# Performance work log

Measured on AMD Instinct MI355X. Metric: run time of the kernel, lower is better.

Reference implementation:

```python
import math
import jax, jax.numpy as jnp
import numpy as np

N_EMBD = 1024
N_HEAD = 16
N_QUERY_SETS = 4
B, T = 8, 1024


def setup_inputs() -> dict:
    key = jax.random.key(0)
    kx, kw1, kw2 = jax.random.split(key, 3)
    C = N_EMBD
    x = jax.random.normal(kx, (B, T, C), dtype=jnp.float32)
    # torch Linear weights are [out_features, in_features]
    W_attn = jax.random.normal(kw1, ((N_QUERY_SETS + 2) * C, C), dtype=jnp.float32) * (1.0 / math.sqrt(C))
    W_proj = jax.random.normal(kw2, (C, N_QUERY_SETS * C), dtype=jnp.float32) * (1.0 / math.sqrt(N_QUERY_SETS * C))
    return {"x": x, "W_attn": W_attn, "W_proj": W_proj}


def reference(x, W_attn, W_proj):
    Bz, Tz, C = x.shape
    hd = C // N_HEAD
    scale = 1.0 / math.sqrt(hd)
    qkv = x @ W_attn.T                       # [B,T,(nqs+2)*C]
    parts = jnp.split(qkv, N_QUERY_SETS + 2, axis=-1)
    k = parts[-2].reshape(Bz, Tz, N_HEAD, hd).transpose(0, 2, 1, 3)  # [B,H,T,hd]
    v = parts[-1].reshape(Bz, Tz, N_HEAD, hd).transpose(0, 2, 1, 3)
    causal = jnp.tril(jnp.ones((Tz, Tz), dtype=bool))
    outs = []
    for g in range(N_QUERY_SETS):  # fixed small structural loop, reuses K/V
        q = parts[g].reshape(Bz, Tz, N_HEAD, hd).transpose(0, 2, 1, 3)
        att = jnp.einsum('bhqd,bhkd->bhqk', q, k) * scale
        att = jnp.where(causal, att, -jnp.inf)
        att = jax.nn.softmax(att, axis=-1)
        y = jnp.einsum('bhqk,bhkd->bhqd', att, v)
        outs.append(y.transpose(0, 2, 1, 3).reshape(Bz, Tz, C))
    combined = jnp.concatenate(outs, axis=-1)  # [B,T,nqs*C]
    return combined @ W_proj.T                 # [B,T,C]
```

## Files before the change

kernel.cpp:

```cpp
#include <hip/hip_runtime.h>


#define DEVI __device__ __forceinline__

typedef __attribute__((ext_vector_type(4)))  float f32x4;
typedef __attribute__((ext_vector_type(16))) float f32x16;
typedef __attribute__((ext_vector_type(8)))  short bf16x8;

static DEVI short f2bf(float f) {
    union { float f; unsigned int i; } c; c.f = f;
    unsigned int i = c.i;
    unsigned int r = i + 0x7FFFu + ((i >> 16) & 1u);
    return (short)(r >> 16);
}

static DEVI unsigned pk2bf(float a, float b) {
    return __builtin_amdgcn_perm(__float_as_uint(b), __float_as_uint(a), 0x07060302u);
}

static DEVI void gload16(const void* g, void* l) {
    __builtin_amdgcn_global_load_lds(
        (const __attribute__((address_space(1))) unsigned int*)g,
        (__attribute__((address_space(3))) unsigned int*)l,
        16, 0, 0);
}

#define BARRIER() do { __builtin_amdgcn_s_barrier(); \
                       __builtin_amdgcn_sched_barrier(0); } while (0)
#define WAITVM(n) do { asm volatile("s_waitcnt vmcnt(%0)" :: "i"(n) : "memory"); \
                       __builtin_amdgcn_sched_barrier(0); } while (0)

__global__ __launch_bounds__(256)
void cvt_all(const float* __restrict__ x, const float* __restrict__ Wa,
             short* __restrict__ dst, float qs) {
    const int i = blockIdx.x * 256 + threadIdx.x;
    const int X8 = 1048576, WQ8 = 524288;
    const float* src;
    float scale = 1.0f;
    if (i < X8) {
        src = x + (size_t)i * 8;
    } else {
        int j = i - X8;
        src = Wa + (size_t)j * 8;
        if (j < WQ8) scale = qs;
    }
    const float4* p = (const float4*)src;
    float4 v0 = p[0], v1 = p[1];
    short r[8] = { f2bf(v0.x * scale), f2bf(v0.y * scale),
                   f2bf(v0.z * scale), f2bf(v0.w * scale),
                   f2bf(v1.x * scale), f2bf(v1.y * scale),
                   f2bf(v1.z * scale), f2bf(v1.w * scale) };
    *(uint4*)(dst + (size_t)i * 8) = *(uint4*)r;
}

__global__ __launch_bounds__(256)
void cvt_bf16(const float* __restrict__ in, short* __restrict__ out, int n8,
              float scale) {
    int i = blockIdx.x * 256 + threadIdx.x;
    if (i >= n8) return;
    const float4* p = (const float4*)in + (size_t)i * 2;
    float4 v0 = p[0], v1 = p[1];
    short r[8] = { f2bf(v0.x * scale), f2bf(v0.y * scale),
                   f2bf(v0.z * scale), f2bf(v0.w * scale),
                   f2bf(v1.x * scale), f2bf(v1.y * scale),
                   f2bf(v1.z * scale), f2bf(v1.w * scale) };
    *(uint4*)(out + (size_t)i * 8) = *(uint4*)r;
}

static DEVI void stage_half(const short* __restrict__ G, int ldg,
                            short* ldsHalf, int tid) {
    #pragma unroll
    for (int i = 0; i < 2; ++i) {
        int c = tid + (i << 9);
        int row = c >> 3;
        int k8 = (c & 7) ^ (row & 7);
        gload16(G + (size_t)row * ldg + k8 * 8, ldsHalf + ((c >> 6) << 9));
    }
}

static DEVI bf16x8 ldsfrag(const short* half, int lr, int k8r) {
    int off = lr * 64 + ((k8r ^ (lr & 7)) << 3);
    return *(const bf16x8*)(half + off);
}

__global__ __launch_bounds__(512)
void gemm8_bt(const short* __restrict__ A, const short* __restrict__ B,
              short* __restrict__ C, int M, int N, int K, int nwgN) {
    __shared__ short lds[65536];
    short* const ldsA = lds;
    short* const ldsB = lds + 32768;

    const int tid  = threadIdx.x;
    const int lane = tid & 63;
    const int w    = tid >> 6;
    const int wr   = w >> 2;
    const int wc   = w & 3;
    const int l15  = lane & 15;
    const int g4   = lane >> 4;

    const int nwg = gridDim.x;
    const int wg  = blockIdx.x;
    const int swz = (wg & 7) * (nwg >> 3) + (wg >> 3);
    const int tm  = swz / nwgN, tn = swz % nwgN;

    const short* Ag = A + (size_t)tm * 256 * K;
    const short* Bg = B + (size_t)tn * 256 * K;
    const int NT = K >> 6;

    f32x4 acc[8][4] = {};

    stage_half(Ag,                      K, ldsA,               tid);
    stage_half(Ag + (size_t)128 * K,    K, ldsA + 8192,        tid);
    stage_half(Bg,                      K, ldsB,               tid);
    stage_half(Bg + (size_t)128 * K,    K, ldsB + 8192,        tid);
    stage_half(Bg + 64,                 K, ldsB + 16384,       tid);
    stage_half(Bg + (size_t)128 * K + 64, K, ldsB + 16384 + 8192, tid);
    WAITVM(4);
    BARRIER();

    for (int u = 0; u < NT; ++u) {
        const int buf = u & 1;
        const short* Ah = ldsA + buf * 16384 + wr * 8192;
        const short* Bh = ldsB + buf * 16384 + (wc >> 1) * 8192;
        const int lrB = (wc & 1) * 64;
        short* stA = ldsA + (buf ^ 1) * 16384;
        short* stB = ldsB + buf * 16384;
        const short* AgN  = Ag + (size_t)(u + 1) * 64;
        const short* BgN2 = Bg + (size_t)(u + 2) * 64;
        const bool doA = (u + 1 < NT), doB = (u + 2 < NT);

        bf16x8 af[4][2], b0[2][2], b1[2][2];

        #pragma unroll
        for (int f = 0; f < 4; ++f)
            #pragma unroll
            for (int ks = 0; ks < 2; ++ks)
                af[f][ks] = ldsfrag(Ah, f * 16 + l15, ks * 4 + g4);
        #pragma unroll
        for (int fn = 0; fn < 2; ++fn)
            #pragma unroll
            for (int ks = 0; ks < 2; ++ks)
                b0[fn][ks] = ldsfrag(Bh, lrB + fn * 16 + l15, ks * 4 + g4);
        if (doA) stage_half(AgN, K, stA, tid);
        BARRIER();
        __builtin_amdgcn_s_setprio(1);
        #pragma unroll
        for (int f = 0; f < 4; ++f)
            #pragma unroll
            for (int fn = 0; fn < 2; ++fn)
                #pragma unroll
                for (int ks = 0; ks < 2; ++ks)
                    acc[f][fn] = __builtin_amdgcn_mfma_f32_16x16x32_bf16(
                        af[f][ks], b0[fn][ks], acc[f][fn], 0, 0, 0);
        __builtin_amdgcn_s_setprio(0);
        BARRIER();

        #pragma unroll
        for (int fn = 0; fn < 2; ++fn)
            #pragma unroll
            for (int ks = 0; ks < 2; ++ks)
                b1[fn][ks] = ldsfrag(Bh, lrB + 32 + fn * 16 + l15, ks * 4 + g4);
        if (doA) stage_half(AgN + (size_t)128 * K, K, stA + 8192, tid);
        BARRIER();
        __builtin_amdgcn_s_setprio(1);
        #pragma unroll
        for (int f = 0; f < 4; ++f)
            #pragma unroll
            for (int fn = 0; fn < 2; ++fn)
                #pragma unroll
                for (int ks = 0; ks < 2; ++ks)
                    acc[f][2 + fn] = __builtin_amdgcn_mfma_f32_16x16x32_bf16(
                        af[f][ks], b1[fn][ks], acc[f][2 + fn], 0, 0, 0);
        __builtin_amdgcn_s_setprio(0);
        BARRIER();

        #pragma unroll
        for (int f = 0; f < 4; ++f)
            #pragma unroll
            for (int ks = 0; ks < 2; ++ks)
                af[f][ks] = ldsfrag(Ah, 64 + f * 16 + l15, ks * 4 + g4);
        if (doB) stage_half(BgN2, K, stB, tid);
        BARRIER();
        __builtin_amdgcn_s_setprio(1);
        #pragma unroll
        for (int f = 0; f < 4; ++f)
            #pragma unroll
            for (int fn = 0; fn < 2; ++fn)
                #pragma unroll
                for (int ks = 0; ks < 2; ++ks)
                    acc[4 + f][fn] = __builtin_amdgcn_mfma_f32_16x16x32_bf16(
                        af[f][ks], b0[fn][ks], acc[4 + f][fn], 0, 0, 0);
        __builtin_amdgcn_s_setprio(0);
        BARRIER();

        if (doB) stage_half(BgN2 + (size_t)128 * K, K, stB + 8192, tid);
        BARRIER();
        __builtin_amdgcn_s_setprio(1);
        #pragma unroll
        for (int f = 0; f < 4; ++f)
            #pragma unroll
            for (int fn = 0; fn < 2; ++fn)
                #pragma unroll
                for (int ks = 0; ks < 2; ++ks)
                    acc[4 + f][2 + fn] = __builtin_amdgcn_mfma_f32_16x16x32_bf16(
                        af[f][ks], b1[fn][ks], acc[4 + f][2 + fn], 0, 0, 0);
        __builtin_amdgcn_s_setprio(0);
        if (doB) { WAITVM(4); } else { WAITVM(0); }
        BARRIER();
    }

    const size_t r0 = (size_t)tm * 256 + wr * 128 + g4 * 4;
    const int    c0 = tn * 256 + wc * 64 + l15;
    #pragma unroll
    for (int mf = 0; mf < 8; ++mf)
        #pragma unroll
        for (int nf = 0; nf < 4; ++nf)
            #pragma unroll
            for (int j = 0; j < 4; ++j)
                C[(r0 + mf * 16 + j) * N + c0 + nf * 16] = f2bf(acc[mf][nf][j]);
}

__global__ __launch_bounds__(512)
void gemm8_bt2(const short* __restrict__ A, const short* __restrict__ B,
               float* __restrict__ C, int M, int N, int K) {
    __shared__ short lds[49152];
    short* const ldsA = lds;
    short* const ldsB = lds + 32768;

    const int tid  = threadIdx.x;
    const int lane = tid & 63;
    const int w    = tid >> 6;
    const int wr   = w >> 2;
    const int wc   = w & 3;
    const int l15  = lane & 15;
    const int g4   = lane >> 4;

    const int nwg = gridDim.x;
    const int wg  = blockIdx.x;
    const int swz = (wg & 7) * (nwg >> 3) + (wg >> 3);
    const int tm  = swz >> 3, tn = swz & 7;

    const short* Ag = A + (size_t)tm * 256 * K;
    const short* Bg = B + (size_t)tn * 128 * K;
    const int NT = K >> 6;

    f32x4 acc[8][2] = {};

    stage_half(Ag,                   K, ldsA,        tid);
    stage_half(Ag + (size_t)128 * K, K, ldsA + 8192, tid);
    stage_half(Bg,                   K, ldsB,        tid);
    stage_half(Bg + 64,              K, ldsB + 8192, tid);
    WAITVM(2);
    BARRIER();

    for (int u = 0; u < NT; ++u) {
        const int buf = u & 1;
        const short* Ah = ldsA + buf * 16384 + wr * 8192;
        const short* Bb = ldsB + buf * 8192;
        short* stA = ldsA + (buf ^ 1) * 16384;
        short* stB = ldsB + buf * 8192;
        const short* AgN  = Ag + (size_t)(u + 1) * 64;
        const short* BgN2 = Bg + (size_t)(u + 2) * 64;
        const bool doA = (u + 1 < NT), doB = (u + 2 < NT);

        bf16x8 af[4][2], b[2][2];

        #pragma unroll
        for (int f = 0; f < 4; ++f)
            #pragma unroll
            for (int ks = 0; ks < 2; ++ks)
                af[f][ks] = ldsfrag(Ah, f * 16 + l15, ks * 4 + g4);
        #pragma unroll
        for (int fn = 0; fn < 2; ++fn)
            #pragma unroll
            for (int ks = 0; ks < 2; ++ks)
                b[fn][ks] = ldsfrag(Bb, wc * 32 + fn * 16 + l15, ks * 4 + g4);
        if (doA) stage_half(AgN, K, stA, tid);
        BARRIER();
        __builtin_amdgcn_s_setprio(1);
        #pragma unroll
        for (int f = 0; f < 4; ++f)
            #pragma unroll
            for (int fn = 0; fn < 2; ++fn)
                #pragma unroll
                for (int ks = 0; ks < 2; ++ks)
                    acc[f][fn] = __builtin_amdgcn_mfma_f32_16x16x32_bf16(
                        af[f][ks], b[fn][ks], acc[f][fn], 0, 0, 0);
        __builtin_amdgcn_s_setprio(0);
        BARRIER();

        #pragma unroll
        for (int f = 0; f < 4; ++f)
            #pragma unroll
            for (int ks = 0; ks < 2; ++ks)
                af[f][ks] = ldsfrag(Ah, 64 + f * 16 + l15, ks * 4 + g4);
        if (doA) stage_half(AgN + (size_t)128 * K, K, stA + 8192, tid);
        if (doB) stage_half(BgN2, K, stB, tid);
        BARRIER();
        __builtin_amdgcn_s_setprio(1);
        #pragma unroll
        for (int f = 0; f < 4; ++f)
            #pragma unroll
            for (int fn = 0; fn < 2; ++fn)
                #pragma unroll
                for (int ks = 0; ks < 2; ++ks)
                    acc[4 + f][fn] = __builtin_amdgcn_mfma_f32_16x16x32_bf16(
                        af[f][ks], b[fn][ks], acc[4 + f][fn], 0, 0, 0);
        __builtin_amdgcn_s_setprio(0);
        if (doB) { WAITVM(2); } else { WAITVM(0); }
        BARRIER();
    }

    const size_t r0 = (size_t)tm * 256 + wr * 128 + g4 * 4;
    const int    c0 = tn * 128 + wc * 32 + l15;
    #pragma unroll
    for (int mf = 0; mf < 8; ++mf)
        #pragma unroll
        for (int nf = 0; nf < 2; ++nf)
            #pragma unroll
            for (int j = 0; j < 4; ++j)
                C[(r0 + mf * 16 + j) * N + c0 + nf * 16] = acc[mf][nf][j];
}

__global__ __launch_bounds__(512, 4)
void attn_fwd(const short* __restrict__ qkv, short* __restrict__ Y) {
    __shared__ __align__(16) char smem[34816];
    short* const KsB0 = (short*)smem;
    short* const VtB0 = (short*)smem + 4096;
    short* const KsB1 = (short*)smem + 8192;
    short* const VtB1 = (short*)smem + 12288;

    const int tid  = threadIdx.x;
    const int lane = tid & 63;
    const int w    = tid >> 6;
    const int q    = lane & 31;
    const int hf   = lane >> 5;

    const int b  = blockIdx.x >> 4;
    const int h  = blockIdx.x & 15;
    const int qt = (gridDim.y - 1) - blockIdx.y;
    const int g  = w >> 1;
    const int lq = (w & 1) * 32 + q;
    const size_t RS = 6144;
    const int bT = b * 1024;

    bf16x8 qf[4];
    {
        const short* qp = qkv + (size_t)(bT + qt * 64 + lq) * RS + g * 1024 + h * 64 + 8 * hf;
        #pragma unroll
        for (int ks2 = 0; ks2 < 4; ks2++)
            qf[ks2] = *(const bf16x8*)(qp + 16 * ks2);
    }

    f32x16 ot[2] = {};
    float lsum = 0.f;

    const int kvS   = tid >> 3;
    const int klog  = (tid & 7) ^ (kvS & 7);
    const int d2    = tid >> 4;
    const int ch4   = tid & 15;
    const int vd0   = d2 * 2;
    const int vp0   = (ch4 >> 1) ^ (vd0 & 7);
    const int vp1   = (ch4 >> 1) ^ ((vd0 + 1) & 7);

    const short* const kvtile = qkv + (size_t)bT * RS + h * 64;

    {
        const short* vp = kvtile + (size_t)(ch4 * 4) * RS + 5120 + vd0;
        unsigned v0 = *(const unsigned*)(vp);
        unsigned v1 = *(const unsigned*)(vp + RS);
        unsigned v2 = *(const unsigned*)(vp + 2 * RS);
        unsigned v3 = *(const unsigned*)(vp + 3 * RS);
        gload16(kvtile + (size_t)kvS * RS + 4096 + klog * 8, KsB0 + w * 512);
        uint2 lo, hi2;
        lo.x  = __builtin_amdgcn_perm(v1, v0, 0x05040100u);
        lo.y  = __builtin_amdgcn_perm(v3, v2, 0x05040100u);
        hi2.x = __builtin_amdgcn_perm(v1, v0, 0x07060302u);
        hi2.y = __builtin_amdgcn_perm(v3, v2, 0x07060302u);
        char* vb = (char*)VtB0;
        *(uint2*)(vb + vd0 * 128 + vp0 * 16 + (ch4 & 1) * 8)       = lo;
        *(uint2*)(vb + (vd0 + 1) * 128 + vp1 * 16 + (ch4 & 1) * 8) = hi2;
    }
    __syncthreads();

    for (int kvt = 0; kvt <= qt; kvt++) {
        short* const Ksc = (kvt & 1) ? KsB1 : KsB0;
        short* const Vtc = (kvt & 1) ? VtB1 : VtB0;
        short* const Ksn = (kvt & 1) ? KsB0 : KsB1;
        short* const Vtn = (kvt & 1) ? VtB0 : VtB1;
        const bool pf = (kvt < qt);

        unsigned v0, v1, v2, v3;
        if (pf) {
            const short* vp = kvtile + (size_t)((kvt + 1) * 64 + ch4 * 4) * RS + 5120 + vd0;
            v0 = *(const unsigned*)(vp);
            v1 = *(const unsigned*)(vp + RS);
            v2 = *(const unsigned*)(vp + 2 * RS);
            v3 = *(const unsigned*)(vp + 3 * RS);
            gload16(kvtile + (size_t)((kvt + 1) * 64 + kvS) * RS + 4096 + klog * 8,
                    Ksn + w * 512);
        }

        f32x16 stt[2] = {};
        __builtin_amdgcn_s_setprio(1);
        #pragma unroll
        for (int sti = 0; sti < 2; sti++) {
            const int kvr = sti * 32 + q;
            #pragma unroll
            for (int ks2 = 0; ks2 < 4; ks2++) {
                const int phys = (2 * ks2 + hf) ^ (kvr & 7);
                bf16x8 kf = *(const bf16x8*)(Ksc + kvr * 64 + phys * 8);
                stt[sti] = __builtin_amdgcn_mfma_f32_32x32x16_bf16(kf, qf[ks2], stt[sti], 0, 0, 0);
            }
        }
        __builtin_amdgcn_s_setprio(0);

        if (kvt == qt) {
            #pragma unroll
            for (int sti = 0; sti < 2; sti++)
                #pragma unroll
                for (int r = 0; r < 16; r++) {
                    int kvl = sti * 32 + (r & 3) + 8 * (r >> 2) + 4 * hf;
                    if (kvl > lq) stt[sti][r] = -3e38f;
                }
        }

        float sp[4] = { 0.f, 0.f, 0.f, 0.f };
        #pragma unroll
        for (int sti = 0; sti < 2; sti++)
            #pragma unroll
            for (int r = 0; r < 16; r++) {
                float e = __builtin_amdgcn_exp2f(stt[sti][r]);
                stt[sti][r] = e;
                sp[r & 3] += e;
            }
        float sum = (sp[0] + sp[1]) + (sp[2] + sp[3]);
        sum += __shfl_xor(sum, 32);
        lsum += sum;

        if (pf) {
            uint2 lo, hi2;
            lo.x  = __builtin_amdgcn_perm(v1, v0, 0x05040100u);
            lo.y  = __builtin_amdgcn_perm(v3, v2, 0x05040100u);
            hi2.x = __builtin_amdgcn_perm(v1, v0, 0x07060302u);
            hi2.y = __builtin_amdgcn_perm(v3, v2, 0x07060302u);
            char* vb = (char*)Vtn;
            *(uint2*)(vb + vd0 * 128 + vp0 * 16 + (ch4 & 1) * 8)       = lo;
            *(uint2*)(vb + (vd0 + 1) * 128 + vp1 * 16 + (ch4 & 1) * 8) = hi2;
        }

        bf16x8 pf4[4];
        #pragma unroll
        for (int ks = 0; ks < 4; ks++) {
            const int sti = ks >> 1, base = 8 * (ks & 1);
            unsigned X0 = pk2bf(stt[sti][base + 0], stt[sti][base + 1]);
            unsigned X1 = pk2bf(stt[sti][base + 2], stt[sti][base + 3]);
            unsigned Y0 = pk2bf(stt[sti][base + 4], stt[sti][base + 5]);
            unsigned Y1 = pk2bf(stt[sti][base + 6], stt[sti][base + 7]);
            asm("v_permlane32_swap_b32 %0, %1" : "+v"(X0), "+v"(Y0));
            asm("v_permlane32_swap_b32 %0, %1" : "+v"(X1), "+v"(Y1));
            unsigned t[4] = { X0, X1, Y0, Y1 };
            pf4[ks] = *(bf16x8*)t;
        }

        __builtin_amdgcn_s_setprio(1);
        #pragma unroll
        for (int dsub = 0; dsub < 2; dsub++) {
            const int dr = dsub * 32 + q;
            #pragma unroll
            for (int ks = 0; ks < 4; ks++) {
                const int phys = (2 * ks + hf) ^ (dr & 7);
                bf16x8 vf = *(const bf16x8*)(Vtc + dr * 64 + phys * 8);
                ot[dsub] = __builtin_amdgcn_mfma_f32_32x32x16_bf16(vf, pf4[ks], ot[dsub], 0, 0, 0);
            }
        }
        __builtin_amdgcn_s_setprio(0);

        __syncthreads();
    }

    unsigned* obuf = (unsigned*)smem;
    const float inv = 1.0f / lsum;
    const int SQ = g * 64 + lq;
    #pragma unroll
    for (int dsub = 0; dsub < 2; dsub++)
        #pragma unroll
        for (int r = 0; r < 16; r += 2) {
            int d = dsub * 32 + (r & 3) + 8 * (r >> 2) + 4 * hf;
            unsigned pk = ((unsigned)(unsigned short)f2bf(ot[dsub][r] * inv)) |
                          (((unsigned)(unsigned short)f2bf(ot[dsub][r + 1] * inv)) << 16);
            obuf[SQ * 34 + (d >> 1)] = pk;
        }
    __syncthreads();
    {
        const int SQ2 = tid >> 1, seg = tid & 1;
        const int g2 = SQ2 >> 6, lq2 = SQ2 & 63;
        const size_t row = (size_t)(bT + qt * 64 + lq2);
        const unsigned* src = obuf + SQ2 * 34 + seg * 16;
        unsigned* dst = (unsigned*)(Y + row * 4096 + g2 * 1024 + h * 64 + seg * 32);
        #pragma unroll
        for (int k = 0; k < 4; k++) {
            uint2 u0 = *(const uint2*)(src + 4 * k);
            uint2 u1 = *(const uint2*)(src + 4 * k + 2);
            uint4 t; t.x = u0.x; t.y = u0.y; t.z = u1.x; t.w = u1.y;
            *(uint4*)(dst + 4 * k) = t;
        }
    }
}

extern "C" void kernel_launch(void* const* d_in, const int* in_sizes, int n_in,
                              void* d_out, int out_size, void* d_ws, size_t ws_size,
                              hipStream_t stream) {
    const float* x  = (const float*)d_in[0];
    const float* Wa = (const float*)d_in[1];
    const float* Wp = (const float*)d_in[2];
    float* out = (float*)d_out;

    short* qkv = (short*)d_ws;
    short* Yb  = qkv + (size_t)8192 * 6144;
    short* xb  = Yb;
    short* Wab = Yb + (size_t)8192 * 1024;
    short* Wpb = qkv;

    const float QS = 0.18033688011112042f;
    dim3 blk(256);
    cvt_all<<<dim3((8192 + 6144) * 1024 / 8 / 256), blk, 0, stream>>>(x, Wa, xb, QS);
    gemm8_bt<<<dim3(768), dim3(512), 0, stream>>>(xb, Wab, qkv, 8192, 6144, 1024, 24);
    attn_fwd<<<dim3(128, 16), dim3(512), 0, stream>>>(qkv, Yb);
    cvt_bf16<<<dim3(1024 * 4096 / 8 / 256), blk, 0, stream>>>(Wp, Wpb, 1024 * 4096 / 8, 1.0f);
    gemm8_bt2<<<dim3(256), dim3(512), 0, stream>>>(Yb, Wpb, out, 8192, 1024, 4096);
}
```

Baseline: 313.8 us.

## Process two KV tiles per barrier with four-stage LDS ring buffer

Reworks the attention KV loop from double buffering with one barrier per 64-key tile to a 4-slot LDS ring. Two tiles are computed per iteration and the next two are prefetched, which halves the number of __syncthreads calls and gives loads more time to land. The cost is LDS use rising from about 34 KB to 64 KB, which may limit the 4-blocks-per-CU occupancy, and more registers held live for the staged V values.

```diff
diff --git a/kernel.cpp b/kernel.cpp
--- a/kernel.cpp
+++ b/kernel.cpp
@@ -324,11 +324,7 @@
 
 __global__ __launch_bounds__(512, 4)
 void attn_fwd(const short* __restrict__ qkv, short* __restrict__ Y) {
-    __shared__ __align__(16) char smem[34816];
-    short* const KsB0 = (short*)smem;
-    short* const VtB0 = (short*)smem + 4096;
-    short* const KsB1 = (short*)smem + 8192;
-    short* const VtB1 = (short*)smem + 12288;
+    __shared__ __align__(16) char smem[65536];
 
     const int tid  = threadIdx.x;
     const int lane = tid & 63;
@@ -343,6 +339,7 @@
     const int lq = (w & 1) * 32 + q;
     const size_t RS = 6144;
     const int bT = b * 1024;
+    const int NT = qt + 1;
 
     bf16x8 qf[4];
     {
@@ -365,42 +362,33 @@
 
     const short* const kvtile = qkv + (size_t)bT * RS + h * 64;
 
-    {
-        const short* vp = kvtile + (size_t)(ch4 * 4) * RS + 5120 + vd0;
-        unsigned v0 = *(const unsigned*)(vp);
-        unsigned v1 = *(const unsigned*)(vp + RS);
-        unsigned v2 = *(const unsigned*)(vp + 2 * RS);
-        unsigned v3 = *(const unsigned*)(vp + 3 * RS);
-        gload16(kvtile + (size_t)kvS * RS + 4096 + klog * 8, KsB0 + w * 512);
+    auto Ks = [&](int t) { return (short*)smem + (t & 3) * 8192; };
+    auto Vt = [&](int t) { return (short*)smem + (t & 3) * 8192 + 4096; };
+
+    auto kstage = [&](int t) {
+        gload16(kvtile + (size_t)(t * 64 + kvS) * RS + 4096 + klog * 8,
+                Ks(t) + w * 512);
+    };
+    auto vload = [&](int t, unsigned* gg) {
+        const short* vp = kvtile + (size_t)(t * 64 + ch4 * 4) * RS + 5120 + vd0;
+        gg[0] = *(const unsigned*)(vp);
+        gg[1] = *(const unsigned*)(vp + RS);
+        gg[2] = *(const unsigned*)(vp + 2 * RS);
+        gg[3] = *(const unsigned*)(vp + 3 * RS);
+    };
+    auto vwrite = [&](int t, const unsigned* gg) {
         uint2 lo, hi2;
-        lo.x  = __builtin_amdgcn_perm(v1, v0, 0x05040100u);
-        lo.y  = __builtin_amdgcn_perm(v3, v2, 0x05040100u);
-        hi2.x = __builtin_amdgcn_perm(v1, v0, 0x07060302u);
-        hi2.y = __builtin_amdgcn_perm(v3, v2, 0x07060302u);
-        char* vb = (char*)VtB0;
+        lo.x  = __builtin_amdgcn_perm(gg[1], gg[0], 0x05040100u);
+        lo.y  = __builtin_amdgcn_perm(gg[3], gg[2], 0x05040100u);
+        hi2.x = __builtin_amdgcn_perm(gg[1], gg[0], 0x07060302u);
+        hi2.y = __builtin_amdgcn_perm(gg[3], gg[2], 0x07060302u);
+        char* vb = (char*)Vt(t);
         *(uint2*)(vb + vd0 * 128 + vp0 * 16 + (ch4 & 1) * 8)       = lo;
         *(uint2*)(vb + (vd0 + 1) * 128 + vp1 * 16 + (ch4 & 1) * 8) = hi2;
-    }
-    __syncthreads();
-
-    for (int kvt = 0; kvt <= qt; kvt++) {
-        short* const Ksc = (kvt & 1) ? KsB1 : KsB0;
-        short* const Vtc = (kvt & 1) ? VtB1 : VtB0;
-        short* const Ksn = (kvt & 1) ? KsB0 : KsB1;
-        short* const Vtn = (kvt & 1) ? VtB0 : VtB1;
-        const bool pf = (kvt < qt);
-
-        unsigned v0, v1, v2, v3;
-        if (pf) {
-            const short* vp = kvtile + (size_t)((kvt + 1) * 64 + ch4 * 4) * RS + 5120 + vd0;
-            v0 = *(const unsigned*)(vp);
-            v1 = *(const unsigned*)(vp + RS);
-            v2 = *(const unsigned*)(vp + 2 * RS);
-            v3 = *(const unsigned*)(vp + 3 * RS);
-            gload16(kvtile + (size_t)((kvt + 1) * 64 + kvS) * RS + 4096 + klog * 8,
-                    Ksn + w * 512);
-        }
-
+    };
+    auto compute_tile = [&](int t) {
+        const short* Ksc = Ks(t);
+        const short* Vtc = Vt(t);
         f32x16 stt[2] = {};
         __builtin_amdgcn_s_setprio(1);
         #pragma unroll
@@ -415,7 +403,7 @@
         }
         __builtin_amdgcn_s_setprio(0);
 
-        if (kvt == qt) {
+        if (t == qt) {
             #pragma unroll
             for (int sti = 0; sti < 2; sti++)
                 #pragma unroll
@@ -438,17 +426,6 @@
         sum += __shfl_xor(sum, 32);
         lsum += sum;
 
-        if (pf) {
-            uint2 lo, hi2;
-            lo.x  = __builtin_amdgcn_perm(v1, v0, 0x05040100u);
-            lo.y  = __builtin_amdgcn_perm(v3, v2, 0x05040100u);
-            hi2.x = __builtin_amdgcn_perm(v1, v0, 0x07060302u);
-            hi2.y = __builtin_amdgcn_perm(v3, v2, 0x07060302u);
-            char* vb = (char*)Vtn;
-            *(uint2*)(vb + vd0 * 128 + vp0 * 16 + (ch4 & 1) * 8)       = lo;
-            *(uint2*)(vb + (vd0 + 1) * 128 + vp1 * 16 + (ch4 & 1) * 8) = hi2;
-        }
-
         bf16x8 pf4[4];
         #pragma unroll
         for (int ks = 0; ks < 4; ks++) {
@@ -459,8 +436,8 @@
             unsigned Y1 = pk2bf(stt[sti][base + 6], stt[sti][base + 7]);
             asm("v_permlane32_swap_b32 %0, %1" : "+v"(X0), "+v"(Y0));
             asm("v_permlane32_swap_b32 %0, %1" : "+v"(X1), "+v"(Y1));
-            unsigned t[4] = { X0, X1, Y0, Y1 };
-            pf4[ks] = *(bf16x8*)t;
+            unsigned tt[4] = { X0, X1, Y0, Y1 };
+            pf4[ks] = *(bf16x8*)tt;
         }
 
         __builtin_amdgcn_s_setprio(1);
@@ -475,7 +452,32 @@
             }
         }
         __builtin_amdgcn_s_setprio(0);
-
+    };
+
+    {
+        unsigned g0[4];
+        vload(0, g0);
+        kstage(0);
+        vwrite(0, g0);
+        if (NT > 1) {
+            unsigned g1[4];
+            vload(1, g1);
+            kstage(1);
+            vwrite(1, g1);
+        }
+    }
+    __syncthreads();
+
+    for (int s = 0; s < NT; s += 2) {
+        const bool pf2 = (s + 2 < NT), pf3 = (s + 3 < NT), hasT1 = (s + 1 < NT);
+        unsigned ga[4], gb[4];
+        if (pf2) { vload(s + 2, ga); kstage(s + 2); }
+        if (pf3) kstage(s + 3);
+        compute_tile(s);
+        if (pf3) vload(s + 3, gb);
+        if (pf2) vwrite(s + 2, ga);
+        if (hasT1) compute_tile(s + 1);
+        if (pf3) vwrite(s + 3, gb);
         __syncthreads();
     }
 
```

New measurement: 321.3 us. +2.4%, slower.
